# Performance work log

Measured on AMD Instinct MI355X. Metric: run time of the kernel, lower is better.

The kernel has to match this reference:

```python
import jax, jax.numpy as jnp
import numpy as np

D_MODEL = 1024
NUM_HEADS = 16
D_K = D_MODEL // NUM_HEADS
LOCAL_WINDOW = 3
STRIDE = 4


def strided_mask(seq_len):
    # position i attends to j iff j <= i and (i-j <= local_window or (i-j) % stride == 0)
    i = jnp.arange(seq_len)[:, None]
    j = jnp.arange(seq_len)[None, :]
    d = i - j
    return (d >= 0) & ((d <= LOCAL_WINDOW) | (d % STRIDE == 0))


def setup_inputs() -> dict:
    key = jax.random.key(0)
    ks = jax.random.split(key, 11)
    B, S, D = 4, 1024, D_MODEL
    s = 1.0 / np.sqrt(D)
    inp = {
        "Q": jax.random.normal(ks[0], (B, S, D), jnp.float32),
        "K": jax.random.normal(ks[1], (B, S, D), jnp.float32),
        "V": jax.random.normal(ks[2], (B, S, D), jnp.float32),
        "Wq": jax.random.normal(ks[3], (D, D), jnp.float32) * s,
        "bq": jnp.zeros((D,), jnp.float32),
        "Wk": jax.random.normal(ks[4], (D, D), jnp.float32) * s,
        "bk": jnp.zeros((D,), jnp.float32),
        "Wv": jax.random.normal(ks[5], (D, D), jnp.float32) * s,
        "bv": jnp.zeros((D,), jnp.float32),
        "Wo": jax.random.normal(ks[6], (D, D), jnp.float32) * s,
        "bo": jnp.zeros((D,), jnp.float32),
    }
    return inp


def reference(Q, K, V, Wq, bq, Wk, bk, Wv, bv, Wo, bo):
    B, S, D = Q.shape
    H, dk = NUM_HEADS, D_K

    def split(x):  # [B,S,D] -> [B,H,S,dk]
        return x.reshape(B, S, H, dk).transpose(0, 2, 1, 3)

    q = split(Q @ Wq + bq)
    k = split(K @ Wk + bk)
    v = split(V @ Wv + bv)

    scores = jnp.einsum("bhsd,bhtd->bhst", q, k) / jnp.sqrt(
        jnp.asarray(dk, jnp.float32))
    m = strided_mask(S)[None, None]  # [1,1,S,S]
    scores = jnp.where(m, scores, -1e9)
    attn = jax.nn.softmax(scores, axis=-1)
    out = jnp.einsum("bhst,bhtd->bhsd", attn, v)
    out = out.transpose(0, 2, 1, 3).reshape(B, S, D)  # combine heads
    return out @ Wo + bo
```

## Files before the change

### kernel.cpp

```cpp
#include <hip/hip_runtime.h>

typedef _Float16 f16;
typedef __attribute__((ext_vector_type(8))) _Float16 f16x8;
typedef __attribute__((ext_vector_type(4))) _Float16 f16x4;
typedef __attribute__((ext_vector_type(4))) float f32x4;

#define MFMA16(a, b, c) __builtin_amdgcn_mfma_f32_16x16x32_f16((a), (b), (c), 0, 0, 0)

__device__ __forceinline__ void gld_lds16(const void* g, void* l) {
  __builtin_amdgcn_global_load_lds(
      (__attribute__((address_space(1))) void*)const_cast<void*>(g),
      (__attribute__((address_space(3))) void*)l, 16, 0, 0);
}

__device__ __forceinline__ f16x8 ld8(const f16* p) { return *(const f16x8*)p; }

__global__ __launch_bounds__(256) void cvt_x_kernel(
    const float* __restrict__ Q, const float* __restrict__ K, const float* __restrict__ V,
    f16* __restrict__ oq, f16* __restrict__ ok, f16* __restrict__ ov) {
  const float* src = blockIdx.z == 0 ? Q : (blockIdx.z == 1 ? K : V);
  f16* dst = blockIdx.z == 0 ? oq : (blockIdx.z == 1 ? ok : ov);
  size_t i = ((size_t)blockIdx.x * 256 + threadIdx.x) * 4;
  float4 f = *(const float4*)(src + i);
  f16x4 o4;
  o4.x = (f16)f.x; o4.y = (f16)f.y; o4.z = (f16)f.z; o4.w = (f16)f.w;
  *(f16x4*)(dst + i) = o4;
}

__global__ __launch_bounds__(256) void cvt_wT_kernel(
    const float* __restrict__ Wq, const float* __restrict__ Wk,
    const float* __restrict__ Wv, const float* __restrict__ Wo,
    f16* __restrict__ Tq, f16* __restrict__ Tk, f16* __restrict__ Tv, f16* __restrict__ To) {
  const int z = blockIdx.z;
  const float* W = z == 0 ? Wq : (z == 1 ? Wk : (z == 2 ? Wv : Wo));
  f16* T = z == 0 ? Tq : (z == 1 ? Tk : (z == 2 ? Tv : To));
  __shared__ float tile[64][65];
  const int k0 = blockIdx.x * 64, n0 = blockIdx.y * 64;
  const int tx = threadIdx.x & 63, ty = threadIdx.x >> 6;
#pragma unroll
  for (int rr = 0; rr < 16; ++rr) {
    int r = rr * 4 + ty;
    tile[r][tx] = W[(size_t)(k0 + r) * 1024 + n0 + tx];
  }
  __syncthreads();
#pragma unroll
  for (int rr = 0; rr < 16; ++rr) {
    int nn = rr * 4 + ty;
    T[(size_t)(n0 + nn) * 1024 + k0 + tx] = (f16)tile[tx][nn];
  }
}

template <bool QKV>
__global__ __launch_bounds__(256) void gemm_bt_kernel(
    const f16* __restrict__ A0, const f16* __restrict__ A1, const f16* __restrict__ A2,
    const f16* __restrict__ B0, const f16* __restrict__ B1, const f16* __restrict__ B2,
    const float* __restrict__ bias0, const float* __restrict__ bias1, const float* __restrict__ bias2,
    f16* __restrict__ C0, f16* __restrict__ C1, f16* __restrict__ C2,
    f16* __restrict__ C3, float* __restrict__ Cf) {
  const int z = blockIdx.z;
  const f16* A = z == 0 ? A0 : (z == 1 ? A1 : A2);
  const f16* Bt = z == 0 ? B0 : (z == 1 ? B1 : B2);
  const float* bias = z == 0 ? bias0 : (z == 1 ? bias1 : bias2);

  __shared__ alignas(16) f16 lA[128 * 32];
  __shared__ alignas(16) f16 lB[128 * 32];

  const int t = threadIdx.x;
  const int w = t >> 6, lane = t & 63, quad = lane >> 4, l15 = lane & 15;
  const int wm = w >> 1, wn = w & 1;
  const int mbase = blockIdx.x * 128;
  const int nbase = blockIdx.y * 128;

  const f32x4 zero4 = {0.f, 0.f, 0.f, 0.f};
  f32x4 acc[4][4];
#pragma unroll
  for (int mi = 0; mi < 4; ++mi)
#pragma unroll
    for (int ni = 0; ni < 4; ++ni) acc[mi][ni] = zero4;

  const int r = t >> 2;
  const int koff = (t & 3) * 8;

  for (int k0 = 0; k0 < 1024; k0 += 32) {
    __syncthreads();
    gld_lds16(A + (size_t)(mbase + r) * 1024 + k0 + koff, (char*)lA + w * 1024);
    gld_lds16(A + (size_t)(mbase + 64 + r) * 1024 + k0 + koff, (char*)lA + 4096 + w * 1024);
    gld_lds16(Bt + (size_t)(nbase + r) * 1024 + k0 + koff, (char*)lB + w * 1024);
    gld_lds16(Bt + (size_t)(nbase + 64 + r) * 1024 + k0 + koff, (char*)lB + 4096 + w * 1024);
    __syncthreads();

    f16x8 af[4], bf[4];
#pragma unroll
    for (int mi = 0; mi < 4; ++mi)
      af[mi] = ld8(&lA[(wm * 64 + mi * 16 + l15) * 32 + quad * 8]);
#pragma unroll
    for (int ni = 0; ni < 4; ++ni)
      bf[ni] = ld8(&lB[(wn * 64 + ni * 16 + l15) * 32 + quad * 8]);
#pragma unroll
    for (int mi = 0; mi < 4; ++mi)
#pragma unroll
      for (int ni = 0; ni < 4; ++ni)
        acc[mi][ni] = MFMA16(af[mi], bf[ni], acc[mi][ni]);
  }

#pragma unroll
  for (int mi = 0; mi < 4; ++mi) {
#pragma unroll
    for (int ni = 0; ni < 4; ++ni) {
#pragma unroll
      for (int rg = 0; rg < 4; ++rg) {
        const int row = mbase + wm * 64 + mi * 16 + quad * 4 + rg;
        const int col = nbase + wn * 64 + ni * 16 + l15;
        const float v = acc[mi][ni][rg] + bias[col];
        if (QKV) {
          const int bh = (row >> 10) * 16 + (col >> 6);
          const int s = row & 1023, d = col & 63;
          const f16 hv = (f16)v;
          if (z != 2) {
            f16* Ch = (z == 0) ? C0 : C1;
            Ch[(size_t)bh * 65536 + s * 64 + d] = hv;
          } else {
            C2[(size_t)bh * 65536 + s * 64 + d] = hv;
            const int rr = s & 3, n = s >> 2, wi = n & 63;
            C3[(size_t)bh * 65536 + (size_t)rr * 16384 + (size_t)d * 256 +
               (n & ~63) + ((wi & 15) << 2) + (wi >> 4)] = hv;
          }
        } else {
          Cf[(size_t)row * 1024 + col] = v;
        }
      }
    }
  }
}

__global__ __launch_bounds__(256) void gemm_out_kernel(
    const f16* __restrict__ A, const f16* __restrict__ Bt,
    const float* __restrict__ bias, float* __restrict__ Cf) {
  __shared__ alignas(16) f16 lA[64 * 32];
  __shared__ alignas(16) f16 lB[128 * 32];

  const int t = threadIdx.x;
  const int w = t >> 6, lane = t & 63, quad = lane >> 4, l15 = lane & 15;
  const int wm = w >> 1, wn = w & 1;
  const int mbase = blockIdx.x * 64;
  const int nbase = blockIdx.y * 128;

  const f32x4 zero4 = {0.f, 0.f, 0.f, 0.f};
  f32x4 acc[2][4];
#pragma unroll
  for (int mi = 0; mi < 2; ++mi)
#pragma unroll
    for (int ni = 0; ni < 4; ++ni) acc[mi][ni] = zero4;

  const int r = t >> 2;
  const int koff = (t & 3) * 8;

  for (int k0 = 0; k0 < 1024; k0 += 32) {
    __syncthreads();
    gld_lds16(A + (size_t)(mbase + r) * 1024 + k0 + koff, (char*)lA + w * 1024);
    gld_lds16(Bt + (size_t)(nbase + r) * 1024 + k0 + koff, (char*)lB + w * 1024);
    gld_lds16(Bt + (size_t)(nbase + 64 + r) * 1024 + k0 + koff, (char*)lB + 4096 + w * 1024);
    __syncthreads();

    f16x8 af[2], bf[4];
#pragma unroll
    for (int mi = 0; mi < 2; ++mi)
      af[mi] = ld8(&lA[(wm * 32 + mi * 16 + l15) * 32 + quad * 8]);
#pragma unroll
    for (int ni = 0; ni < 4; ++ni)
      bf[ni] = ld8(&lB[(wn * 64 + ni * 16 + l15) * 32 + quad * 8]);
#pragma unroll
    for (int mi = 0; mi < 2; ++mi)
#pragma unroll
      for (int ni = 0; ni < 4; ++ni)
        acc[mi][ni] = MFMA16(af[mi], bf[ni], acc[mi][ni]);
  }

#pragma unroll
  for (int mi = 0; mi < 2; ++mi)
#pragma unroll
    for (int ni = 0; ni < 4; ++ni)
#pragma unroll
      for (int rg = 0; rg < 4; ++rg) {
        const int row = mbase + wm * 32 + mi * 16 + quad * 4 + rg;
        const int col = nbase + wn * 64 + ni * 16 + l15;
        Cf[(size_t)row * 1024 + col] = acc[mi][ni][rg] + bias[col];
      }
}

__global__ __launch_bounds__(256) void attn_far_kernel(
    const f16* __restrict__ qh, const f16* __restrict__ kh,
    const f16* __restrict__ vtg, float* __restrict__ po, float* __restrict__ ml) {
  const int t = threadIdx.x;
  const int w = t >> 6, lane = t & 63, quad = lane >> 4, l15 = lane & 15;
  const int widx = blockIdx.x + 512 * w;
  const int bh = (widx & 255) >> 2, r = widx & 3;
  const int wq = widx >> 8;
  const int m0 = wq * 32;
  const int ntiles = (wq >> 1) + 1;

  __shared__ alignas(16) f16 lp[4][2][16 * 72];

  const f16* qb = qh + (size_t)bh * 65536;
  const f16* kb = kh + (size_t)bh * 65536;
  const f16* vb = vtg + (size_t)bh * 65536 + (size_t)r * 16384;
  const float SCL2 = 0.125f * 1.44269504f;

  f16x8 aq[2][2];
#pragma unroll
  for (int mt = 0; mt < 2; ++mt) {
    const int i = 4 * (m0 + mt * 16 + l15) + r;
#pragma unroll
    for (int ko = 0; ko < 2; ++ko)
      aq[mt][ko] = ld8(qb + (size_t)i * 64 + ko * 32 + quad * 8);
  }

  const f32x4 zero4 = {0.f, 0.f, 0.f, 0.f};
  f32x4 o[2][4];
  float mrun[2][4], lrun[2][4];
#pragma unroll
  for (int mt = 0; mt < 2; ++mt)
#pragma unroll
    for (int i = 0; i < 4; ++i) {
      o[mt][i] = zero4; mrun[mt][i] = -1e30f; lrun[mt][i] = 0.f;
    }

  for (int jt = 0; jt < ntiles; ++jt) {
    const int n0 = jt * 64;
    f16x8 bk0[4], bk1[4], bv0[4], bv1[4];
#pragma unroll
    for (int nt = 0; nt < 4; ++nt) {
      const f16* kr = kb + (size_t)(4 * (n0 + nt * 16 + l15) + r) * 64;
      bk0[nt] = ld8(kr + quad * 8);
      bk1[nt] = ld8(kr + 32 + quad * 8);
      const f16* vr = vb + (size_t)(nt * 16 + l15) * 256 + n0;
      bv0[nt] = ld8(vr + quad * 8);
      bv1[nt] = ld8(vr + 32 + quad * 8);
    }
    const bool lastt = (jt == ntiles - 1);
#pragma unroll
    for (int mt = 0; mt < 2; ++mt) {
      f32x4 sc[4];
#pragma unroll
      for (int nt = 0; nt < 4; ++nt) {
        f32x4 c = MFMA16(aq[mt][0], bk0[nt], zero4);
        sc[nt] = MFMA16(aq[mt][1], bk1[nt], c);
      }
#pragma unroll
      for (int rg = 0; rg < 4; ++rg) {
        const int m = m0 + mt * 16 + quad * 4 + rg;
        float s[4];
#pragma unroll
        for (int nt = 0; nt < 4; ++nt) {
          float vsc = sc[nt][rg] * SCL2;
          if (lastt) vsc = (n0 + nt * 16 + l15 < m) ? vsc : -3.0e38f;
          s[nt] = vsc;
        }
        float tm = fmaxf(fmaxf(s[0], s[1]), fmaxf(s[2], s[3]));
        tm = fmaxf(tm, __shfl_xor(tm, 1));
        tm = fmaxf(tm, __shfl_xor(tm, 2));
        tm = fmaxf(tm, __shfl_xor(tm, 4));
        tm = fmaxf(tm, __shfl_xor(tm, 8));
        const float mnew = fmaxf(mrun[mt][rg], tm);
        const float alpha = exp2f(mrun[mt][rg] - mnew);
        float p[4], ps = 0.f;
#pragma unroll
        for (int nt = 0; nt < 4; ++nt) { p[nt] = exp2f(s[nt] - mnew); ps += p[nt]; }
        ps += __shfl_xor(ps, 1);
        ps += __shfl_xor(ps, 2);
        ps += __shfl_xor(ps, 4);
        ps += __shfl_xor(ps, 8);
        lrun[mt][rg] = lrun[mt][rg] * alpha + ps;
        mrun[mt][rg] = mnew;
#pragma unroll
        for (int ntv = 0; ntv < 4; ++ntv) o[mt][ntv][rg] *= alpha;
        f16x4 pk;
        pk.x = (f16)p[0]; pk.y = (f16)p[1]; pk.z = (f16)p[2]; pk.w = (f16)p[3];
        *(f16x4*)&lp[w][mt][(quad * 4 + rg) * 72 + l15 * 4] = pk;
      }
    }
#pragma unroll
    for (int mt = 0; mt < 2; ++mt) {
      const f16x8 ap0 = ld8(&lp[w][mt][l15 * 72 + quad * 8]);
      const f16x8 ap1 = ld8(&lp[w][mt][l15 * 72 + 32 + quad * 8]);
#pragma unroll
      for (int ntv = 0; ntv < 4; ++ntv) {
        f32x4 c = MFMA16(ap0, bv0[ntv], o[mt][ntv]);
        o[mt][ntv] = MFMA16(ap1, bv1[ntv], c);
      }
    }
  }

#pragma unroll
  for (int mt = 0; mt < 2; ++mt)
#pragma unroll
    for (int rg = 0; rg < 4; ++rg) {
      const int i = 4 * (m0 + mt * 16 + quad * 4 + rg) + r;
      const size_t idx = (size_t)bh * 1024 + i;
#pragma unroll
      for (int ntv = 0; ntv < 4; ++ntv)
        po[idx * 64 + ntv * 16 + l15] = o[mt][ntv][rg];
      if (l15 == 0) { ml[idx * 2] = mrun[mt][rg]; ml[idx * 2 + 1] = lrun[mt][rg]; }
    }
}

__global__ __launch_bounds__(256) void attn_diag_kernel(
    const f16* __restrict__ qh, const f16* __restrict__ kh, const f16* __restrict__ vh,
    const float* __restrict__ po, const float* __restrict__ ml, f16* __restrict__ ao) {
  const int t = threadIdx.x;
  const int widx = blockIdx.x * 4 + (t >> 6);
  const int l = t & 63;
  const int bh = widx >> 10, i = widx & 1023;
  const float SCL2 = 0.125f * 1.44269504f;

  const float q = (float)qh[(size_t)bh * 65536 + (size_t)i * 64 + l];
  float s[4];
#pragma unroll
  for (int d = 0; d < 4; ++d) {
    const int j = i - d;
    const int jc = j < 0 ? 0 : j;
    float pr = q * (float)kh[(size_t)bh * 65536 + (size_t)jc * 64 + l];
    pr += __shfl_xor(pr, 1);
    pr += __shfl_xor(pr, 2);
    pr += __shfl_xor(pr, 4);
    pr += __shfl_xor(pr, 8);
    pr += __shfl_xor(pr, 16);
    pr += __shfl_xor(pr, 32);
    s[d] = (j >= 0) ? pr * SCL2 : -3.0e38f;
  }
  const float md = fmaxf(fmaxf(s[0], s[1]), fmaxf(s[2], s[3]));
  const size_t idx = (size_t)bh * 1024 + i;
  const float mf = ml[idx * 2], lf = ml[idx * 2 + 1];
  const float M = fmaxf(md, mf);
  float p[4], ld = 0.f;
#pragma unroll
  for (int d = 0; d < 4; ++d) { p[d] = exp2f(s[d] - M); ld += p[d]; }
  float ov = 0.f;
#pragma unroll
  for (int d = 0; d < 4; ++d) {
    const int jc = (i - d) < 0 ? 0 : (i - d);
    ov += p[d] * (float)vh[(size_t)bh * 65536 + (size_t)jc * 64 + l];
  }
  const float fs = exp2f(mf - M);
  const float lt = lf * fs + ld;
  const float of = po[idx * 64 + l];
  const float res = (of * fs + ov) / lt;
  const int b = bh >> 4, h = bh & 15;
  ao[((size_t)(b * 1024 + i)) * 1024 + h * 64 + l] = (f16)res;
}

extern "C" void kernel_launch(void* const* d_in, const int* in_sizes, int n_in,
                              void* d_out, int out_size, void* d_ws, size_t ws_size,
                              hipStream_t stream) {
  const float* Q = (const float*)d_in[0];
  const float* K = (const float*)d_in[1];
  const float* V = (const float*)d_in[2];
  const float* Wq = (const float*)d_in[3];
  const float* bq = (const float*)d_in[4];
  const float* Wk = (const float*)d_in[5];
  const float* bk = (const float*)d_in[6];
  const float* Wv = (const float*)d_in[7];
  const float* bv = (const float*)d_in[8];
  const float* Wo = (const float*)d_in[9];
  const float* bo = (const float*)d_in[10];
  float* out = (float*)d_out;

  char* ws = (char*)d_ws;
  const size_t MB = 1ull << 20;
  f16* Xq  = (f16*)(ws + 0 * MB);
  f16* Xk  = (f16*)(ws + 8 * MB);
  f16* Xv  = (f16*)(ws + 16 * MB);
  f16* TWq = (f16*)(ws + 24 * MB);
  f16* TWk = (f16*)(ws + 26 * MB);
  f16* TWv = (f16*)(ws + 28 * MB);
  f16* TWo = (f16*)(ws + 30 * MB);
  f16* qhb = (f16*)(ws + 32 * MB);
  f16* khb = (f16*)(ws + 40 * MB);
  f16* vhb = (f16*)(ws + 48 * MB);
  f16* vtg = (f16*)(ws + 56 * MB);
  float* po  = (float*)(ws + 0 * MB);
  float* mlb = (float*)(ws + 16 * MB);
  f16* aob   = (f16*)(ws + 17 * MB);

  cvt_x_kernel<<<dim3(4096, 1, 3), 256, 0, stream>>>(Q, K, V, Xq, Xk, Xv);
  cvt_wT_kernel<<<dim3(16, 16, 4), 256, 0, stream>>>(Wq, Wk, Wv, Wo, TWq, TWk, TWv, TWo);
  gemm_bt_kernel<true><<<dim3(32, 8, 3), 256, 0, stream>>>(
      Xq, Xk, Xv, TWq, TWk, TWv, bq, bk, bv, qhb, khb, vhb, vtg, nullptr);
  attn_far_kernel<<<dim3(512), 256, 0, stream>>>(qhb, khb, vtg, po, mlb);
  attn_diag_kernel<<<dim3(16384), 256, 0, stream>>>(qhb, khb, vhb, po, mlb, aob);
  gemm_out_kernel<<<dim3(64, 8), 256, 0, stream>>>(aob, TWo, bo, out);
}
```

Measured before the change: 228.3 us.

## Merge conversion kernels, deepen GEMM K-tile with XOR-swizzled LDS, move diagonal term

The two fp16 conversion kernels become one launch, with the weight-transpose blocks packed into the z=3 slice. Both GEMMs load 64-wide K tiles instead of 32, using an XOR-swizzled LDS layout, which halves the number of sync-separated iterations and avoids bank conflicts on the fragment reads. The d=0 diagonal score moves from the diag kernel into the far kernel's masked last tile, so the diag kernel only handles offsets 1..3. The cost is more LDS per block, which may lower occupancy, and the kernel that owns the diagonal term changes.

```diff
diff --git a/kernel.cpp b/kernel.cpp
--- a/kernel.cpp
+++ b/kernel.cpp
@@ -15,27 +15,29 @@
 
 __device__ __forceinline__ f16x8 ld8(const f16* p) { return *(const f16x8*)p; }
 
-__global__ __launch_bounds__(256) void cvt_x_kernel(
+__global__ __launch_bounds__(256) void cvt_all_kernel(
     const float* __restrict__ Q, const float* __restrict__ K, const float* __restrict__ V,
-    f16* __restrict__ oq, f16* __restrict__ ok, f16* __restrict__ ov) {
-  const float* src = blockIdx.z == 0 ? Q : (blockIdx.z == 1 ? K : V);
-  f16* dst = blockIdx.z == 0 ? oq : (blockIdx.z == 1 ? ok : ov);
-  size_t i = ((size_t)blockIdx.x * 256 + threadIdx.x) * 4;
-  float4 f = *(const float4*)(src + i);
-  f16x4 o4;
-  o4.x = (f16)f.x; o4.y = (f16)f.y; o4.z = (f16)f.z; o4.w = (f16)f.w;
-  *(f16x4*)(dst + i) = o4;
-}
-
-__global__ __launch_bounds__(256) void cvt_wT_kernel(
+    f16* __restrict__ oq, f16* __restrict__ ok, f16* __restrict__ ov,
     const float* __restrict__ Wq, const float* __restrict__ Wk,
     const float* __restrict__ Wv, const float* __restrict__ Wo,
     f16* __restrict__ Tq, f16* __restrict__ Tk, f16* __restrict__ Tv, f16* __restrict__ To) {
-  const int z = blockIdx.z;
-  const float* W = z == 0 ? Wq : (z == 1 ? Wk : (z == 2 ? Wv : Wo));
-  f16* T = z == 0 ? Tq : (z == 1 ? Tk : (z == 2 ? Tv : To));
   __shared__ float tile[64][65];
-  const int k0 = blockIdx.x * 64, n0 = blockIdx.y * 64;
+  if (blockIdx.z < 3) {
+    const float* src = blockIdx.z == 0 ? Q : (blockIdx.z == 1 ? K : V);
+    f16* dst = blockIdx.z == 0 ? oq : (blockIdx.z == 1 ? ok : ov);
+    size_t i = ((size_t)blockIdx.x * 256 + threadIdx.x) * 4;
+    float4 f = *(const float4*)(src + i);
+    f16x4 o4;
+    o4.x = (f16)f.x; o4.y = (f16)f.y; o4.z = (f16)f.z; o4.w = (f16)f.w;
+    *(f16x4*)(dst + i) = o4;
+    return;
+  }
+  if (blockIdx.x >= 1024) return;
+  const int zz = blockIdx.x >> 8;
+  const float* W = zz == 0 ? Wq : (zz == 1 ? Wk : (zz == 2 ? Wv : Wo));
+  f16* T = zz == 0 ? Tq : (zz == 1 ? Tk : (zz == 2 ? Tv : To));
+  const int tidx = blockIdx.x & 255;
+  const int k0 = (tidx & 15) * 64, n0 = (tidx >> 4) * 64;
   const int tx = threadIdx.x & 63, ty = threadIdx.x >> 6;
 #pragma unroll
   for (int rr = 0; rr < 16; ++rr) {
@@ -62,8 +64,8 @@
   const f16* Bt = z == 0 ? B0 : (z == 1 ? B1 : B2);
   const float* bias = z == 0 ? bias0 : (z == 1 ? bias1 : bias2);
 
-  __shared__ alignas(16) f16 lA[128 * 32];
-  __shared__ alignas(16) f16 lB[128 * 32];
+  __shared__ alignas(16) f16 lA[128 * 64];
+  __shared__ alignas(16) f16 lB[128 * 64];
 
   const int t = threadIdx.x;
   const int w = t >> 6, lane = t & 63, quad = lane >> 4, l15 = lane & 15;
@@ -78,29 +80,38 @@
 #pragma unroll
     for (int ni = 0; ni < 4; ++ni) acc[mi][ni] = zero4;
 
-  const int r = t >> 2;
-  const int koff = (t & 3) * 8;
-
-  for (int k0 = 0; k0 < 1024; k0 += 32) {
+  const int rsub = t >> 3;
+  const int kswz = ((t & 7) ^ (rsub & 7)) << 3;
+
+  for (int k0 = 0; k0 < 1024; k0 += 64) {
     __syncthreads();
-    gld_lds16(A + (size_t)(mbase + r) * 1024 + k0 + koff, (char*)lA + w * 1024);
-    gld_lds16(A + (size_t)(mbase + 64 + r) * 1024 + k0 + koff, (char*)lA + 4096 + w * 1024);
-    gld_lds16(Bt + (size_t)(nbase + r) * 1024 + k0 + koff, (char*)lB + w * 1024);
-    gld_lds16(Bt + (size_t)(nbase + 64 + r) * 1024 + k0 + koff, (char*)lB + 4096 + w * 1024);
+#pragma unroll
+    for (int c4 = 0; c4 < 4; ++c4) {
+      gld_lds16(A + (size_t)(mbase + c4 * 32 + rsub) * 1024 + k0 + kswz,
+                (char*)lA + c4 * 4096 + w * 1024);
+      gld_lds16(Bt + (size_t)(nbase + c4 * 32 + rsub) * 1024 + k0 + kswz,
+                (char*)lB + c4 * 4096 + w * 1024);
+    }
     __syncthreads();
 
-    f16x8 af[4], bf[4];
-#pragma unroll
-    for (int mi = 0; mi < 4; ++mi)
-      af[mi] = ld8(&lA[(wm * 64 + mi * 16 + l15) * 32 + quad * 8]);
-#pragma unroll
-    for (int ni = 0; ni < 4; ++ni)
-      bf[ni] = ld8(&lB[(wn * 64 + ni * 16 + l15) * 32 + quad * 8]);
-#pragma unroll
-    for (int mi = 0; mi < 4; ++mi)
+    f16x8 af[2][4], bf[2][4];
+#pragma unroll
+    for (int ko = 0; ko < 2; ++ko) {
+      const int pos = (((ko << 2) | quad) ^ (l15 & 7)) << 3;
+#pragma unroll
+      for (int mi = 0; mi < 4; ++mi)
+        af[ko][mi] = ld8(&lA[(wm * 64 + mi * 16 + l15) * 64 + pos]);
 #pragma unroll
       for (int ni = 0; ni < 4; ++ni)
-        acc[mi][ni] = MFMA16(af[mi], bf[ni], acc[mi][ni]);
+        bf[ko][ni] = ld8(&lB[(wn * 64 + ni * 16 + l15) * 64 + pos]);
+    }
+#pragma unroll
+    for (int ko = 0; ko < 2; ++ko)
+#pragma unroll
+      for (int mi = 0; mi < 4; ++mi)
+#pragma unroll
+        for (int ni = 0; ni < 4; ++ni)
+          acc[mi][ni] = MFMA16(af[ko][mi], bf[ko][ni], acc[mi][ni]);
   }
 
 #pragma unroll
@@ -136,8 +147,8 @@
 __global__ __launch_bounds__(256) void gemm_out_kernel(
     const f16* __restrict__ A, const f16* __restrict__ Bt,
     const float* __restrict__ bias, float* __restrict__ Cf) {
-  __shared__ alignas(16) f16 lA[64 * 32];
-  __shared__ alignas(16) f16 lB[128 * 32];
+  __shared__ alignas(16) f16 lA[64 * 64];
+  __shared__ alignas(16) f16 lB[128 * 64];
 
   const int t = threadIdx.x;
   const int w = t >> 6, lane = t & 63, quad = lane >> 4, l15 = lane & 15;
@@ -152,28 +163,37 @@
 #pragma unroll
     for (int ni = 0; ni < 4; ++ni) acc[mi][ni] = zero4;
 
-  const int r = t >> 2;
-  const int koff = (t & 3) * 8;
-
-  for (int k0 = 0; k0 < 1024; k0 += 32) {
+  const int rsub = t >> 3;
+  const int kswz = ((t & 7) ^ (rsub & 7)) << 3;
+
+  for (int k0 = 0; k0 < 1024; k0 += 64) {
     __syncthreads();
-    gld_lds16(A + (size_t)(mbase + r) * 1024 + k0 + koff, (char*)lA + w * 1024);
-    gld_lds16(Bt + (size_t)(nbase + r) * 1024 + k0 + koff, (char*)lB + w * 1024);
-    gld_lds16(Bt + (size_t)(nbase + 64 + r) * 1024 + k0 + koff, (char*)lB + 4096 + w * 1024);
+    gld_lds16(A + (size_t)(mbase + rsub) * 1024 + k0 + kswz, (char*)lA + w * 1024);
+    gld_lds16(A + (size_t)(mbase + 32 + rsub) * 1024 + k0 + kswz, (char*)lA + 4096 + w * 1024);
+#pragma unroll
+    for (int c4 = 0; c4 < 4; ++c4)
+      gld_lds16(Bt + (size_t)(nbase + c4 * 32 + rsub) * 1024 + k0 + kswz,
+                (char*)lB + c4 * 4096 + w * 1024);
     __syncthreads();
 
-    f16x8 af[2], bf[4];
-#pragma unroll
-    for (int mi = 0; mi < 2; ++mi)
-      af[mi] = ld8(&lA[(wm * 32 + mi * 16 + l15) * 32 + quad * 8]);
-#pragma unroll
-    for (int ni = 0; ni < 4; ++ni)
-      bf[ni] = ld8(&lB[(wn * 64 + ni * 16 + l15) * 32 + quad * 8]);
-#pragma unroll
-    for (int mi = 0; mi < 2; ++mi)
+    f16x8 af[2][2], bf[2][4];
+#pragma unroll
+    for (int ko = 0; ko < 2; ++ko) {
+      const int pos = (((ko << 2) | quad) ^ (l15 & 7)) << 3;
+#pragma unroll
+      for (int mi = 0; mi < 2; ++mi)
+        af[ko][mi] = ld8(&lA[(wm * 32 + mi * 16 + l15) * 64 + pos]);
 #pragma unroll
       for (int ni = 0; ni < 4; ++ni)
-        acc[mi][ni] = MFMA16(af[mi], bf[ni], acc[mi][ni]);
+        bf[ko][ni] = ld8(&lB[(wn * 64 + ni * 16 + l15) * 64 + pos]);
+    }
+#pragma unroll
+    for (int ko = 0; ko < 2; ++ko)
+#pragma unroll
+      for (int mi = 0; mi < 2; ++mi)
+#pragma unroll
+        for (int ni = 0; ni < 4; ++ni)
+          acc[mi][ni] = MFMA16(af[ko][mi], bf[ko][ni], acc[mi][ni]);
   }
 
 #pragma unroll
@@ -253,7 +273,7 @@
 #pragma unroll
         for (int nt = 0; nt < 4; ++nt) {
           float vsc = sc[nt][rg] * SCL2;
-          if (lastt) vsc = (n0 + nt * 16 + l15 < m) ? vsc : -3.0e38f;
+          if (lastt) vsc = (n0 + nt * 16 + l15 <= m) ? vsc : -3.0e38f;
           s[nt] = vsc;
         }
         float tm = fmaxf(fmaxf(s[0], s[1]), fmaxf(s[2], s[3]));
@@ -314,9 +334,9 @@
   const float SCL2 = 0.125f * 1.44269504f;
 
   const float q = (float)qh[(size_t)bh * 65536 + (size_t)i * 64 + l];
-  float s[4];
-#pragma unroll
-  for (int d = 0; d < 4; ++d) {
+  float s[3];
+#pragma unroll
+  for (int d = 1; d <= 3; ++d) {
     const int j = i - d;
     const int jc = j < 0 ? 0 : j;
     float pr = q * (float)kh[(size_t)bh * 65536 + (size_t)jc * 64 + l];
@@ -326,20 +346,20 @@
     pr += __shfl_xor(pr, 8);
     pr += __shfl_xor(pr, 16);
     pr += __shfl_xor(pr, 32);
-    s[d] = (j >= 0) ? pr * SCL2 : -3.0e38f;
-  }
-  const float md = fmaxf(fmaxf(s[0], s[1]), fmaxf(s[2], s[3]));
+    s[d - 1] = (j >= 0) ? pr * SCL2 : -3.0e38f;
+  }
+  const float md = fmaxf(fmaxf(s[0], s[1]), s[2]);
   const size_t idx = (size_t)bh * 1024 + i;
   const float mf = ml[idx * 2], lf = ml[idx * 2 + 1];
   const float M = fmaxf(md, mf);
-  float p[4], ld = 0.f;
-#pragma unroll
-  for (int d = 0; d < 4; ++d) { p[d] = exp2f(s[d] - M); ld += p[d]; }
+  float p[3], ld = 0.f;
+#pragma unroll
+  for (int d = 1; d <= 3; ++d) { p[d - 1] = exp2f(s[d - 1] - M); ld += p[d - 1]; }
   float ov = 0.f;
 #pragma unroll
-  for (int d = 0; d < 4; ++d) {
+  for (int d = 1; d <= 3; ++d) {
     const int jc = (i - d) < 0 ? 0 : (i - d);
-    ov += p[d] * (float)vh[(size_t)bh * 65536 + (size_t)jc * 64 + l];
+    ov += p[d - 1] * (float)vh[(size_t)bh * 65536 + (size_t)jc * 64 + l];
   }
   const float fs = exp2f(mf - M);
   const float lt = lf * fs + ld;
@@ -382,8 +402,8 @@
   float* mlb = (float*)(ws + 16 * MB);
   f16* aob   = (f16*)(ws + 17 * MB);
 
-  cvt_x_kernel<<<dim3(4096, 1, 3), 256, 0, stream>>>(Q, K, V, Xq, Xk, Xv);
-  cvt_wT_kernel<<<dim3(16, 16, 4), 256, 0, stream>>>(Wq, Wk, Wv, Wo, TWq, TWk, TWv, TWo);
+  cvt_all_kernel<<<dim3(4096, 1, 4), 256, 0, stream>>>(
+      Q, K, V, Xq, Xk, Xv, Wq, Wk, Wv, Wo, TWq, TWk, TWv, TWo);
   gemm_bt_kernel<true><<<dim3(32, 8, 3), 256, 0, stream>>>(
       Xq, Xk, Xv, TWq, TWk, TWv, bq, bk, bv, qhb, khb, vhb, vtg, nullptr);
   attn_far_kernel<<<dim3(512), 256, 0, stream>>>(qhb, khb, vtg, po, mlb);
```

New measurement: 229.5 us. Within noise of the previous version (+0.5%).

## Merge conversion kernels, use 512-thread GEMM blocks, move diagonal into far pass

Applied to the files above, without the earlier changes.

Fuses the activation cast and weight transpose-cast into one launch, dispatching on blockIdx.z, with a 4096x1x4 grid in which most z=3 blocks exit immediately. Both GEMMs move to 8 waves per block, so each wave owns a 64x32 (or 32x32) sub-tile. Each thread now issues fewer global-to-LDS loads and holds fewer accumulators, which should raise occupancy. The far-attention kernel's last-tile mask now includes the diagonal, and the diag kernel drops d=0, cutting one dot product per row. The launch adds many idle blocks, and smaller per-wave tiles lower MFMA reuse per LDS read.

```diff
diff --git a/kernel.cpp b/kernel.cpp
--- a/kernel.cpp
+++ b/kernel.cpp
@@ -15,27 +15,29 @@
 
 __device__ __forceinline__ f16x8 ld8(const f16* p) { return *(const f16x8*)p; }
 
-__global__ __launch_bounds__(256) void cvt_x_kernel(
+__global__ __launch_bounds__(256) void cvt_all_kernel(
     const float* __restrict__ Q, const float* __restrict__ K, const float* __restrict__ V,
-    f16* __restrict__ oq, f16* __restrict__ ok, f16* __restrict__ ov) {
-  const float* src = blockIdx.z == 0 ? Q : (blockIdx.z == 1 ? K : V);
-  f16* dst = blockIdx.z == 0 ? oq : (blockIdx.z == 1 ? ok : ov);
-  size_t i = ((size_t)blockIdx.x * 256 + threadIdx.x) * 4;
-  float4 f = *(const float4*)(src + i);
-  f16x4 o4;
-  o4.x = (f16)f.x; o4.y = (f16)f.y; o4.z = (f16)f.z; o4.w = (f16)f.w;
-  *(f16x4*)(dst + i) = o4;
-}
-
-__global__ __launch_bounds__(256) void cvt_wT_kernel(
+    f16* __restrict__ oq, f16* __restrict__ ok, f16* __restrict__ ov,
     const float* __restrict__ Wq, const float* __restrict__ Wk,
     const float* __restrict__ Wv, const float* __restrict__ Wo,
     f16* __restrict__ Tq, f16* __restrict__ Tk, f16* __restrict__ Tv, f16* __restrict__ To) {
-  const int z = blockIdx.z;
-  const float* W = z == 0 ? Wq : (z == 1 ? Wk : (z == 2 ? Wv : Wo));
-  f16* T = z == 0 ? Tq : (z == 1 ? Tk : (z == 2 ? Tv : To));
   __shared__ float tile[64][65];
-  const int k0 = blockIdx.x * 64, n0 = blockIdx.y * 64;
+  if (blockIdx.z < 3) {
+    const float* src = blockIdx.z == 0 ? Q : (blockIdx.z == 1 ? K : V);
+    f16* dst = blockIdx.z == 0 ? oq : (blockIdx.z == 1 ? ok : ov);
+    size_t i = ((size_t)blockIdx.x * 256 + threadIdx.x) * 4;
+    float4 f = *(const float4*)(src + i);
+    f16x4 o4;
+    o4.x = (f16)f.x; o4.y = (f16)f.y; o4.z = (f16)f.z; o4.w = (f16)f.w;
+    *(f16x4*)(dst + i) = o4;
+    return;
+  }
+  if (blockIdx.x >= 1024) return;
+  const int zz = blockIdx.x >> 8;
+  const float* W = zz == 0 ? Wq : (zz == 1 ? Wk : (zz == 2 ? Wv : Wo));
+  f16* T = zz == 0 ? Tq : (zz == 1 ? Tk : (zz == 2 ? Tv : To));
+  const int tidx = blockIdx.x & 255;
+  const int k0 = (tidx & 15) * 64, n0 = (tidx >> 4) * 64;
   const int tx = threadIdx.x & 63, ty = threadIdx.x >> 6;
 #pragma unroll
   for (int rr = 0; rr < 16; ++rr) {
@@ -51,7 +53,7 @@
 }
 
 template <bool QKV>
-__global__ __launch_bounds__(256) void gemm_bt_kernel(
+__global__ __launch_bounds__(512, 4) void gemm_bt_kernel(
     const f16* __restrict__ A0, const f16* __restrict__ A1, const f16* __restrict__ A2,
     const f16* __restrict__ B0, const f16* __restrict__ B1, const f16* __restrict__ B2,
     const float* __restrict__ bias0, const float* __restrict__ bias1, const float* __restrict__ bias2,
@@ -67,16 +69,16 @@
 
   const int t = threadIdx.x;
   const int w = t >> 6, lane = t & 63, quad = lane >> 4, l15 = lane & 15;
-  const int wm = w >> 1, wn = w & 1;
+  const int wm = w >> 2, wn = w & 3;
   const int mbase = blockIdx.x * 128;
   const int nbase = blockIdx.y * 128;
 
   const f32x4 zero4 = {0.f, 0.f, 0.f, 0.f};
-  f32x4 acc[4][4];
+  f32x4 acc[4][2];
 #pragma unroll
   for (int mi = 0; mi < 4; ++mi)
 #pragma unroll
-    for (int ni = 0; ni < 4; ++ni) acc[mi][ni] = zero4;
+    for (int ni = 0; ni < 2; ++ni) acc[mi][ni] = zero4;
 
   const int r = t >> 2;
   const int koff = (t & 3) * 8;
@@ -84,33 +86,31 @@
   for (int k0 = 0; k0 < 1024; k0 += 32) {
     __syncthreads();
     gld_lds16(A + (size_t)(mbase + r) * 1024 + k0 + koff, (char*)lA + w * 1024);
-    gld_lds16(A + (size_t)(mbase + 64 + r) * 1024 + k0 + koff, (char*)lA + 4096 + w * 1024);
     gld_lds16(Bt + (size_t)(nbase + r) * 1024 + k0 + koff, (char*)lB + w * 1024);
-    gld_lds16(Bt + (size_t)(nbase + 64 + r) * 1024 + k0 + koff, (char*)lB + 4096 + w * 1024);
     __syncthreads();
 
-    f16x8 af[4], bf[4];
+    f16x8 af[4], bf[2];
 #pragma unroll
     for (int mi = 0; mi < 4; ++mi)
       af[mi] = ld8(&lA[(wm * 64 + mi * 16 + l15) * 32 + quad * 8]);
 #pragma unroll
-    for (int ni = 0; ni < 4; ++ni)
-      bf[ni] = ld8(&lB[(wn * 64 + ni * 16 + l15) * 32 + quad * 8]);
+    for (int ni = 0; ni < 2; ++ni)
+      bf[ni] = ld8(&lB[(wn * 32 + ni * 16 + l15) * 32 + quad * 8]);
 #pragma unroll
     for (int mi = 0; mi < 4; ++mi)
 #pragma unroll
-      for (int ni = 0; ni < 4; ++ni)
+      for (int ni = 0; ni < 2; ++ni)
         acc[mi][ni] = MFMA16(af[mi], bf[ni], acc[mi][ni]);
   }
 
 #pragma unroll
   for (int mi = 0; mi < 4; ++mi) {
 #pragma unroll
-    for (int ni = 0; ni < 4; ++ni) {
+    for (int ni = 0; ni < 2; ++ni) {
 #pragma unroll
       for (int rg = 0; rg < 4; ++rg) {
         const int row = mbase + wm * 64 + mi * 16 + quad * 4 + rg;
-        const int col = nbase + wn * 64 + ni * 16 + l15;
+        const int col = nbase + wn * 32 + ni * 16 + l15;
         const float v = acc[mi][ni][rg] + bias[col];
         if (QKV) {
           const int bh = (row >> 10) * 16 + (col >> 6);
@@ -133,7 +133,7 @@
   }
 }
 
-__global__ __launch_bounds__(256) void gemm_out_kernel(
+__global__ __launch_bounds__(512, 4) void gemm_out_kernel(
     const f16* __restrict__ A, const f16* __restrict__ Bt,
     const float* __restrict__ bias, float* __restrict__ Cf) {
   __shared__ alignas(16) f16 lA[64 * 32];
@@ -141,49 +141,49 @@
 
   const int t = threadIdx.x;
   const int w = t >> 6, lane = t & 63, quad = lane >> 4, l15 = lane & 15;
-  const int wm = w >> 1, wn = w & 1;
+  const int wm = w >> 2, wn = w & 3;
   const int mbase = blockIdx.x * 64;
   const int nbase = blockIdx.y * 128;
 
   const f32x4 zero4 = {0.f, 0.f, 0.f, 0.f};
-  f32x4 acc[2][4];
+  f32x4 acc[2][2];
 #pragma unroll
   for (int mi = 0; mi < 2; ++mi)
 #pragma unroll
-    for (int ni = 0; ni < 4; ++ni) acc[mi][ni] = zero4;
+    for (int ni = 0; ni < 2; ++ni) acc[mi][ni] = zero4;
 
   const int r = t >> 2;
   const int koff = (t & 3) * 8;
 
   for (int k0 = 0; k0 < 1024; k0 += 32) {
     __syncthreads();
-    gld_lds16(A + (size_t)(mbase + r) * 1024 + k0 + koff, (char*)lA + w * 1024);
+    if (w < 4)
+      gld_lds16(A + (size_t)(mbase + r) * 1024 + k0 + koff, (char*)lA + w * 1024);
     gld_lds16(Bt + (size_t)(nbase + r) * 1024 + k0 + koff, (char*)lB + w * 1024);
-    gld_lds16(Bt + (size_t)(nbase + 64 + r) * 1024 + k0 + koff, (char*)lB + 4096 + w * 1024);
     __syncthreads();
 
-    f16x8 af[2], bf[4];
+    f16x8 af[2], bf[2];
 #pragma unroll
     for (int mi = 0; mi < 2; ++mi)
       af[mi] = ld8(&lA[(wm * 32 + mi * 16 + l15) * 32 + quad * 8]);
 #pragma unroll
-    for (int ni = 0; ni < 4; ++ni)
-      bf[ni] = ld8(&lB[(wn * 64 + ni * 16 + l15) * 32 + quad * 8]);
+    for (int ni = 0; ni < 2; ++ni)
+      bf[ni] = ld8(&lB[(wn * 32 + ni * 16 + l15) * 32 + quad * 8]);
 #pragma unroll
     for (int mi = 0; mi < 2; ++mi)
 #pragma unroll
-      for (int ni = 0; ni < 4; ++ni)
+      for (int ni = 0; ni < 2; ++ni)
         acc[mi][ni] = MFMA16(af[mi], bf[ni], acc[mi][ni]);
   }
 
 #pragma unroll
   for (int mi = 0; mi < 2; ++mi)
 #pragma unroll
-    for (int ni = 0; ni < 4; ++ni)
+    for (int ni = 0; ni < 2; ++ni)
 #pragma unroll
       for (int rg = 0; rg < 4; ++rg) {
         const int row = mbase + wm * 32 + mi * 16 + quad * 4 + rg;
-        const int col = nbase + wn * 64 + ni * 16 + l15;
+        const int col = nbase + wn * 32 + ni * 16 + l15;
         Cf[(size_t)row * 1024 + col] = acc[mi][ni][rg] + bias[col];
       }
 }
@@ -253,7 +253,7 @@
 #pragma unroll
         for (int nt = 0; nt < 4; ++nt) {
           float vsc = sc[nt][rg] * SCL2;
-          if (lastt) vsc = (n0 + nt * 16 + l15 < m) ? vsc : -3.0e38f;
+          if (lastt) vsc = (n0 + nt * 16 + l15 <= m) ? vsc : -3.0e38f;
           s[nt] = vsc;
         }
         float tm = fmaxf(fmaxf(s[0], s[1]), fmaxf(s[2], s[3]));
@@ -314,9 +314,9 @@
   const float SCL2 = 0.125f * 1.44269504f;
 
   const float q = (float)qh[(size_t)bh * 65536 + (size_t)i * 64 + l];
-  float s[4];
-#pragma unroll
-  for (int d = 0; d < 4; ++d) {
+  float s[3];
+#pragma unroll
+  for (int d = 1; d <= 3; ++d) {
     const int j = i - d;
     const int jc = j < 0 ? 0 : j;
     float pr = q * (float)kh[(size_t)bh * 65536 + (size_t)jc * 64 + l];
@@ -326,20 +326,20 @@
     pr += __shfl_xor(pr, 8);
     pr += __shfl_xor(pr, 16);
     pr += __shfl_xor(pr, 32);
-    s[d] = (j >= 0) ? pr * SCL2 : -3.0e38f;
-  }
-  const float md = fmaxf(fmaxf(s[0], s[1]), fmaxf(s[2], s[3]));
+    s[d - 1] = (j >= 0) ? pr * SCL2 : -3.0e38f;
+  }
+  const float md = fmaxf(fmaxf(s[0], s[1]), s[2]);
   const size_t idx = (size_t)bh * 1024 + i;
   const float mf = ml[idx * 2], lf = ml[idx * 2 + 1];
   const float M = fmaxf(md, mf);
-  float p[4], ld = 0.f;
-#pragma unroll
-  for (int d = 0; d < 4; ++d) { p[d] = exp2f(s[d] - M); ld += p[d]; }
+  float p[3], ld = 0.f;
+#pragma unroll
+  for (int d = 1; d <= 3; ++d) { p[d - 1] = exp2f(s[d - 1] - M); ld += p[d - 1]; }
   float ov = 0.f;
 #pragma unroll
-  for (int d = 0; d < 4; ++d) {
+  for (int d = 1; d <= 3; ++d) {
     const int jc = (i - d) < 0 ? 0 : (i - d);
-    ov += p[d] * (float)vh[(size_t)bh * 65536 + (size_t)jc * 64 + l];
+    ov += p[d - 1] * (float)vh[(size_t)bh * 65536 + (size_t)jc * 64 + l];
   }
   const float fs = exp2f(mf - M);
   const float lt = lf * fs + ld;
@@ -382,11 +382,11 @@
   float* mlb = (float*)(ws + 16 * MB);
   f16* aob   = (f16*)(ws + 17 * MB);
 
-  cvt_x_kernel<<<dim3(4096, 1, 3), 256, 0, stream>>>(Q, K, V, Xq, Xk, Xv);
-  cvt_wT_kernel<<<dim3(16, 16, 4), 256, 0, stream>>>(Wq, Wk, Wv, Wo, TWq, TWk, TWv, TWo);
-  gemm_bt_kernel<true><<<dim3(32, 8, 3), 256, 0, stream>>>(
+  cvt_all_kernel<<<dim3(4096, 1, 4), 256, 0, stream>>>(
+      Q, K, V, Xq, Xk, Xv, Wq, Wk, Wv, Wo, TWq, TWk, TWv, TWo);
+  gemm_bt_kernel<true><<<dim3(32, 8, 3), 512, 0, stream>>>(
       Xq, Xk, Xv, TWq, TWk, TWv, bq, bk, bv, qhb, khb, vhb, vtg, nullptr);
   attn_far_kernel<<<dim3(512), 256, 0, stream>>>(qhb, khb, vtg, po, mlb);
   attn_diag_kernel<<<dim3(16384), 256, 0, stream>>>(qhb, khb, vhb, po, mlb, aob);
-  gemm_out_kernel<<<dim3(64, 8), 256, 0, stream>>>(aob, TWo, bo, out);
-}
+  gemm_out_kernel<<<dim3(64, 8), 512, 0, stream>>>(aob, TWo, bo, out);
+}
```

Result: no change. 230.8 us (+1.1%).

## Merge convert kernels, stage QKV epilogue through LDS, shift diagonal split

Applied to the files above, without the earlier changes.

Merges the activation-convert and weight-transpose kernels into one launch, which removes a kernel launch. In the QKV GEMM, the per-head outputs are now staged through LDS and written as coalesced 16-byte stores instead of scattered 2-byte stores. The transposed V layout is still written with scattered stores. The far-attention kernel now handles the j==i diagonal entry, so the diagonal kernel only computes three local dot products instead of four. The merged launch wastes 3072 blocks that return immediately, and the epilogue adds a barrier and extra LDS traffic.

```diff
diff --git a/kernel.cpp b/kernel.cpp
--- a/kernel.cpp
+++ b/kernel.cpp
@@ -15,27 +15,29 @@
 
 __device__ __forceinline__ f16x8 ld8(const f16* p) { return *(const f16x8*)p; }
 
-__global__ __launch_bounds__(256) void cvt_x_kernel(
+__global__ __launch_bounds__(256) void cvt_all_kernel(
     const float* __restrict__ Q, const float* __restrict__ K, const float* __restrict__ V,
-    f16* __restrict__ oq, f16* __restrict__ ok, f16* __restrict__ ov) {
-  const float* src = blockIdx.z == 0 ? Q : (blockIdx.z == 1 ? K : V);
-  f16* dst = blockIdx.z == 0 ? oq : (blockIdx.z == 1 ? ok : ov);
-  size_t i = ((size_t)blockIdx.x * 256 + threadIdx.x) * 4;
-  float4 f = *(const float4*)(src + i);
-  f16x4 o4;
-  o4.x = (f16)f.x; o4.y = (f16)f.y; o4.z = (f16)f.z; o4.w = (f16)f.w;
-  *(f16x4*)(dst + i) = o4;
-}
-
-__global__ __launch_bounds__(256) void cvt_wT_kernel(
+    f16* __restrict__ oq, f16* __restrict__ ok, f16* __restrict__ ov,
     const float* __restrict__ Wq, const float* __restrict__ Wk,
     const float* __restrict__ Wv, const float* __restrict__ Wo,
     f16* __restrict__ Tq, f16* __restrict__ Tk, f16* __restrict__ Tv, f16* __restrict__ To) {
-  const int z = blockIdx.z;
-  const float* W = z == 0 ? Wq : (z == 1 ? Wk : (z == 2 ? Wv : Wo));
-  f16* T = z == 0 ? Tq : (z == 1 ? Tk : (z == 2 ? Tv : To));
   __shared__ float tile[64][65];
-  const int k0 = blockIdx.x * 64, n0 = blockIdx.y * 64;
+  if (blockIdx.z < 3) {
+    const float* src = blockIdx.z == 0 ? Q : (blockIdx.z == 1 ? K : V);
+    f16* dst = blockIdx.z == 0 ? oq : (blockIdx.z == 1 ? ok : ov);
+    size_t i = ((size_t)blockIdx.x * 256 + threadIdx.x) * 4;
+    float4 f = *(const float4*)(src + i);
+    f16x4 o4;
+    o4.x = (f16)f.x; o4.y = (f16)f.y; o4.z = (f16)f.z; o4.w = (f16)f.w;
+    *(f16x4*)(dst + i) = o4;
+    return;
+  }
+  if (blockIdx.x >= 1024) return;
+  const int zz = blockIdx.x >> 8;
+  const float* W = zz == 0 ? Wq : (zz == 1 ? Wk : (zz == 2 ? Wv : Wo));
+  f16* T = zz == 0 ? Tq : (zz == 1 ? Tk : (zz == 2 ? Tv : To));
+  const int tidx = blockIdx.x & 255;
+  const int k0 = (tidx & 15) * 64, n0 = (tidx >> 4) * 64;
   const int tx = threadIdx.x & 63, ty = threadIdx.x >> 6;
 #pragma unroll
   for (int rr = 0; rr < 16; ++rr) {
@@ -62,8 +64,9 @@
   const f16* Bt = z == 0 ? B0 : (z == 1 ? B1 : B2);
   const float* bias = z == 0 ? bias0 : (z == 1 ? bias1 : bias2);
 
-  __shared__ alignas(16) f16 lA[128 * 32];
-  __shared__ alignas(16) f16 lB[128 * 32];
+  __shared__ alignas(16) char lsm[16384];
+  f16* lA = (f16*)lsm;
+  f16* lB = (f16*)(lsm + 8192);
 
   const int t = threadIdx.x;
   const int w = t >> 6, lane = t & 63, quad = lane >> 4, l15 = lane & 15;
@@ -103,33 +106,56 @@
         acc[mi][ni] = MFMA16(af[mi], bf[ni], acc[mi][ni]);
   }
 
-#pragma unroll
-  for (int mi = 0; mi < 4; ++mi) {
-#pragma unroll
-    for (int ni = 0; ni < 4; ++ni) {
-#pragma unroll
-      for (int rg = 0; rg < 4; ++rg) {
-        const int row = mbase + wm * 64 + mi * 16 + quad * 4 + rg;
-        const int col = nbase + wn * 64 + ni * 16 + l15;
-        const float v = acc[mi][ni][rg] + bias[col];
-        if (QKV) {
-          const int bh = (row >> 10) * 16 + (col >> 6);
-          const int s = row & 1023, d = col & 63;
-          const f16 hv = (f16)v;
-          if (z != 2) {
-            f16* Ch = (z == 0) ? C0 : C1;
-            Ch[(size_t)bh * 65536 + s * 64 + d] = hv;
-          } else {
-            C2[(size_t)bh * 65536 + s * 64 + d] = hv;
+  __syncthreads();
+  const int colbase = nbase + wn * 64;
+  const int rowbase = mbase + wm * 64;
+  if (QKV) {
+    const int bh = (rowbase >> 10) * 16 + (colbase >> 6);
+    const int s0 = rowbase & 1023;
+    f16* eb = (f16*)(lsm + w * 4096);
+    f16* Ch = (z == 0) ? C0 : (z == 1 ? C1 : C2);
+#pragma unroll
+    for (int mi = 0; mi < 4; ++mi) {
+#pragma unroll
+      for (int ni = 0; ni < 4; ++ni)
+#pragma unroll
+        for (int rg = 0; rg < 4; ++rg)
+          eb[(quad * 4 + rg) * 68 + ni * 16 + l15] =
+              (f16)(acc[mi][ni][rg] + bias[colbase + ni * 16 + l15]);
+#pragma unroll
+      for (int j = 0; j < 2; ++j) {
+        const int lr = (lane >> 3) + 8 * j, c8 = lane & 7;
+        const f16x8 vv = ld8(&eb[lr * 68 + c8 * 8]);
+        *(f16x8*)(Ch + (size_t)bh * 65536 +
+                  (size_t)(s0 + mi * 16 + lr) * 64 + c8 * 8) = vv;
+      }
+    }
+    if (z == 2) {
+#pragma unroll
+      for (int mi = 0; mi < 4; ++mi)
+#pragma unroll
+        for (int ni = 0; ni < 4; ++ni)
+#pragma unroll
+          for (int rg = 0; rg < 4; ++rg) {
+            const int s = s0 + mi * 16 + quad * 4 + rg;
+            const int d = ni * 16 + l15;
+            const f16 hv = (f16)(acc[mi][ni][rg] + bias[colbase + d]);
             const int rr = s & 3, n = s >> 2, wi = n & 63;
             C3[(size_t)bh * 65536 + (size_t)rr * 16384 + (size_t)d * 256 +
                (n & ~63) + ((wi & 15) << 2) + (wi >> 4)] = hv;
           }
-        } else {
-          Cf[(size_t)row * 1024 + col] = v;
+    }
+  } else {
+#pragma unroll
+    for (int mi = 0; mi < 4; ++mi)
+#pragma unroll
+      for (int ni = 0; ni < 4; ++ni)
+#pragma unroll
+        for (int rg = 0; rg < 4; ++rg) {
+          const int row = rowbase + mi * 16 + quad * 4 + rg;
+          const int col = colbase + ni * 16 + l15;
+          Cf[(size_t)row * 1024 + col] = acc[mi][ni][rg] + bias[col];
         }
-      }
-    }
   }
 }
 
@@ -253,7 +279,7 @@
 #pragma unroll
         for (int nt = 0; nt < 4; ++nt) {
           float vsc = sc[nt][rg] * SCL2;
-          if (lastt) vsc = (n0 + nt * 16 + l15 < m) ? vsc : -3.0e38f;
+          if (lastt) vsc = (n0 + nt * 16 + l15 <= m) ? vsc : -3.0e38f;
           s[nt] = vsc;
         }
         float tm = fmaxf(fmaxf(s[0], s[1]), fmaxf(s[2], s[3]));
@@ -314,9 +340,9 @@
   const float SCL2 = 0.125f * 1.44269504f;
 
   const float q = (float)qh[(size_t)bh * 65536 + (size_t)i * 64 + l];
-  float s[4];
-#pragma unroll
-  for (int d = 0; d < 4; ++d) {
+  float s[3];
+#pragma unroll
+  for (int d = 1; d <= 3; ++d) {
     const int j = i - d;
     const int jc = j < 0 ? 0 : j;
     float pr = q * (float)kh[(size_t)bh * 65536 + (size_t)jc * 64 + l];
@@ -326,20 +352,20 @@
     pr += __shfl_xor(pr, 8);
     pr += __shfl_xor(pr, 16);
     pr += __shfl_xor(pr, 32);
-    s[d] = (j >= 0) ? pr * SCL2 : -3.0e38f;
-  }
-  const float md = fmaxf(fmaxf(s[0], s[1]), fmaxf(s[2], s[3]));
+    s[d - 1] = (j >= 0) ? pr * SCL2 : -3.0e38f;
+  }
+  const float md = fmaxf(fmaxf(s[0], s[1]), s[2]);
   const size_t idx = (size_t)bh * 1024 + i;
   const float mf = ml[idx * 2], lf = ml[idx * 2 + 1];
   const float M = fmaxf(md, mf);
-  float p[4], ld = 0.f;
-#pragma unroll
-  for (int d = 0; d < 4; ++d) { p[d] = exp2f(s[d] - M); ld += p[d]; }
+  float p[3], ld = 0.f;
+#pragma unroll
+  for (int d = 1; d <= 3; ++d) { p[d - 1] = exp2f(s[d - 1] - M); ld += p[d - 1]; }
   float ov = 0.f;
 #pragma unroll
-  for (int d = 0; d < 4; ++d) {
+  for (int d = 1; d <= 3; ++d) {
     const int jc = (i - d) < 0 ? 0 : (i - d);
-    ov += p[d] * (float)vh[(size_t)bh * 65536 + (size_t)jc * 64 + l];
+    ov += p[d - 1] * (float)vh[(size_t)bh * 65536 + (size_t)jc * 64 + l];
   }
   const float fs = exp2f(mf - M);
   const float lt = lf * fs + ld;
@@ -382,8 +408,8 @@
   float* mlb = (float*)(ws + 16 * MB);
   f16* aob   = (f16*)(ws + 17 * MB);
 
-  cvt_x_kernel<<<dim3(4096, 1, 3), 256, 0, stream>>>(Q, K, V, Xq, Xk, Xv);
-  cvt_wT_kernel<<<dim3(16, 16, 4), 256, 0, stream>>>(Wq, Wk, Wv, Wo, TWq, TWk, TWv, TWo);
+  cvt_all_kernel<<<dim3(4096, 1, 4), 256, 0, stream>>>(
+      Q, K, V, Xq, Xk, Xv, Wq, Wk, Wv, Wo, TWq, TWk, TWv, TWo);
   gemm_bt_kernel<true><<<dim3(32, 8, 3), 256, 0, stream>>>(
       Xq, Xk, Xv, TWq, TWk, TWv, bq, bk, bv, qhb, khb, vhb, vtg, nullptr);
   attn_far_kernel<<<dim3(512), 256, 0, stream>>>(qhb, khb, vtg, po, mlb);
```

New measurement: 224.4 us. Within noise of the previous version (-1.7%).
